# Kernel optimization log

Hardware: AMD Instinct MI355X
Metric: run time of the kernel (lower is better)

The kernel has to match this reference:

```python
import jax, jax.numpy as jnp
import numpy as np

N_NODES = 8192
N_EDGES = 262144


def spmm(edge_index, edge_weight, h):
    # sparse adjacency (COO) times dense matrix: out[dst] += w * h[src]
    src = edge_index[0]
    dst = edge_index[1]
    msg = h[src] * edge_weight[:, None]          # [E, D]
    return jax.ops.segment_sum(msg, dst, num_segments=N_NODES)


def setup_inputs() -> dict:
    key = jax.random.key(0)
    k = jax.random.split(key, 6)
    x = jax.random.normal(k[0], (N_NODES, 512), dtype=jnp.float32)
    edge_index = jax.random.randint(k[1], (2, N_EDGES), 0, N_NODES, dtype=jnp.int64)
    edge_weight = jax.random.uniform(k[2], (N_EDGES,), dtype=jnp.float32)
    # Glorot-style init scale for the GCN weights
    W1 = jax.random.normal(k[3], (512, 256), dtype=jnp.float32) * (1.0 / np.sqrt(512))
    W2 = jax.random.normal(k[4], (256, 128), dtype=jnp.float32) * (1.0 / np.sqrt(256))
    W3 = jax.random.normal(k[5], (256, 128), dtype=jnp.float32) * (1.0 / np.sqrt(256))
    return {"x": x, "edge_index": edge_index, "edge_weight": edge_weight,
            "W1": W1, "W2": W2, "W3": W3}


def reference(x, edge_index, edge_weight, W1, W2, W3):
    # Eval mode: dropout = identity, reparameterize returns mu.
    # GCN layer 1: relu(adj @ (x @ W1))
    h1 = jax.nn.relu(spmm(edge_index, edge_weight, x @ W1))       # [N, 256]
    # GCN layers 2/3 (identity activation): mu, logvar
    mu = spmm(edge_index, edge_weight, h1 @ W2)                   # [N, 128]
    logvar = spmm(edge_index, edge_weight, h1 @ W3)               # [N, 128]
    z = mu                                                        # eval: z = mu
    # InnerProductDecoder with act = identity
    adj_recon = z @ z.T                                           # [N, N]
    return adj_recon, mu, logvar, z
```

## Files before the change

kernel.cpp:

```cpp
#include <hip/hip_runtime.h>
#include <hip/hip_bf16.h>

#define NN 8192
#define NE 262144

typedef __attribute__((ext_vector_type(8))) short bf16x8;
typedef __attribute__((ext_vector_type(4))) float f32x4;
typedef __attribute__((ext_vector_type(16))) float f32x16;
typedef unsigned short u16;
typedef __attribute__((ext_vector_type(4))) u16 u16x4;

__device__ inline u16 f2b(float f) {
  unsigned u = __float_as_uint(f);
  unsigned r = u + 0x7FFF + ((u >> 16) & 1);
  return (u16)(r >> 16);
}
__device__ inline float b2f(u16 b) {
  return __uint_as_float(((unsigned)b) << 16);
}

__global__ void prep_kernel(const float* __restrict__ x, const float* __restrict__ W1,
                            const float* __restrict__ W2, const float* __restrict__ W3,
                            u16* __restrict__ xh, u16* __restrict__ xl,
                            u16* __restrict__ W1h, u16* __restrict__ W1l,
                            u16* __restrict__ W23h, u16* __restrict__ W23l) {
  int b = blockIdx.x;
  if (b < 4096) {
    int i = (b * 256 + threadIdx.x) * 4;
    f32x4 v = *(const f32x4*)(x + i);
    u16x4 vh, vl;
#pragma unroll
    for (int j = 0; j < 4; ++j) {
      u16 h = f2b(v[j]);
      vh[j] = h;
      vl[j] = f2b(v[j] - b2f(h));
    }
    *(u16x4*)(xh + i) = vh;
    *(u16x4*)(xl + i) = vl;
  } else if (b < 4096 + 512) {
    int i = (b - 4096) * 256 + threadIdx.x;
    int k = i >> 8, n = i & 255;
    float v = W1[i];
    u16 h = f2b(v);
    W1h[(size_t)n * 512 + k] = h;
    W1l[(size_t)n * 512 + k] = f2b(v - b2f(h));
  } else {
    int i = (b - 4608) * 256 + threadIdx.x;
    int k = i >> 8, j = i & 255;
    float v = (j < 128) ? W2[(k << 7) + j] : W3[(k << 7) + (j - 128)];
    u16 h = f2b(v);
    W23h[(size_t)j * 256 + k] = h;
    W23l[(size_t)j * 256 + k] = f2b(v - b2f(h));
  }
}

__global__ void hist_kernel(const int* __restrict__ dst, int* __restrict__ deg) {
  int i = blockIdx.x * blockDim.x + threadIdx.x;
  if (i < NE) atomicAdd(&deg[dst[i]], 1);
}

__global__ void scan_kernel(const int* __restrict__ deg, int* __restrict__ rowptr,
                            int* __restrict__ cursor) {
  __shared__ int sums[1024];
  int t = threadIdx.x;
  int loc[8];
  int s = 0;
#pragma unroll
  for (int j = 0; j < 8; ++j) { s += deg[t * 8 + j]; loc[j] = s; }
  sums[t] = s;
  __syncthreads();
  for (int off = 1; off < 1024; off <<= 1) {
    int v = (t >= off) ? sums[t - off] : 0;
    __syncthreads();
    sums[t] += v;
    __syncthreads();
  }
  int base = (t > 0) ? sums[t - 1] : 0;
  if (t == 0) rowptr[0] = 0;
#pragma unroll
  for (int j = 0; j < 8; ++j) {
    rowptr[t * 8 + j + 1] = base + loc[j];
    cursor[t * 8 + j] = base + (j ? loc[j - 1] : 0);
  }
}

__global__ void scatter_kernel(const int* __restrict__ src, const int* __restrict__ dst,
                               const float* __restrict__ w, int* cursor,
                               int* __restrict__ csr_src, float* __restrict__ csr_w) {
  int i = blockIdx.x * blockDim.x + threadIdx.x;
  if (i >= NE) return;
  int d = dst[i];
  int p = atomicAdd(&cursor[d], 1);
  csr_src[p] = src[i];
  csr_w[p] = w[i];
}

__global__ void gemm_split_kernel(const u16* __restrict__ Ah, const u16* __restrict__ Al,
                                  const u16* __restrict__ Bh, const u16* __restrict__ Bl,
                                  u16* __restrict__ C, int M, int N, int K) {
  int wave = threadIdx.x >> 6, lane = threadIdx.x & 63;
  int r = lane & 15, kf = (lane >> 4) * 8;
  int row = blockIdx.x * 64 + wave * 16 + r;
  int col0 = blockIdx.y * 64;
  f32x4 acc[4] = {};
  for (int k0 = 0; k0 < K; k0 += 32) {
    int ka = k0 + kf;
    bf16x8 ah = *(const bf16x8*)(Ah + (size_t)row * K + ka);
    bf16x8 al = *(const bf16x8*)(Al + (size_t)row * K + ka);
#pragma unroll
    for (int t = 0; t < 4; ++t) {
      int col = col0 + t * 16 + r;
      bf16x8 bh = *(const bf16x8*)(Bh + (size_t)col * K + ka);
      bf16x8 bl = *(const bf16x8*)(Bl + (size_t)col * K + ka);
      acc[t] = __builtin_amdgcn_mfma_f32_16x16x32_bf16(ah, bh, acc[t], 0, 0, 0);
      acc[t] = __builtin_amdgcn_mfma_f32_16x16x32_bf16(al, bh, acc[t], 0, 0, 0);
      acc[t] = __builtin_amdgcn_mfma_f32_16x16x32_bf16(ah, bl, acc[t], 0, 0, 0);
    }
  }
  int orow = blockIdx.x * 64 + wave * 16 + (lane >> 4) * 4;
#pragma unroll
  for (int t = 0; t < 4; ++t)
#pragma unroll
    for (int q = 0; q < 4; ++q)
      C[(size_t)(orow + q) * N + col0 + t * 16 + r] = f2b(acc[t][q]);
}

__global__ void spmm_relu_kernel(const int* __restrict__ rowptr, const int* __restrict__ csr_src,
                                 const float* __restrict__ csr_w, const u16* __restrict__ h,
                                 u16* __restrict__ oh, u16* __restrict__ ol) {
  int n = blockIdx.x * 4 + (threadIdx.x >> 6);
  int c = (threadIdx.x & 63) * 4;
  int e0 = rowptr[n], e1 = rowptr[n + 1];
  f32x4 acc = {};
  int i = e0;
  for (; i + 4 <= e1; i += 4) {
    int s0 = csr_src[i], s1 = csr_src[i + 1], s2 = csr_src[i + 2], s3 = csr_src[i + 3];
    float w0 = csr_w[i], w1 = csr_w[i + 1], w2 = csr_w[i + 2], w3 = csr_w[i + 3];
    u16x4 v0 = *(const u16x4*)(h + (size_t)s0 * 256 + c);
    u16x4 v1 = *(const u16x4*)(h + (size_t)s1 * 256 + c);
    u16x4 v2 = *(const u16x4*)(h + (size_t)s2 * 256 + c);
    u16x4 v3 = *(const u16x4*)(h + (size_t)s3 * 256 + c);
#pragma unroll
    for (int j = 0; j < 4; ++j) {
      acc[j] = fmaf(w0, b2f(v0[j]), acc[j]);
      acc[j] = fmaf(w1, b2f(v1[j]), acc[j]);
      acc[j] = fmaf(w2, b2f(v2[j]), acc[j]);
      acc[j] = fmaf(w3, b2f(v3[j]), acc[j]);
    }
  }
  for (; i < e1; ++i) {
    float w0 = csr_w[i];
    u16x4 v0 = *(const u16x4*)(h + (size_t)csr_src[i] * 256 + c);
#pragma unroll
    for (int j = 0; j < 4; ++j) acc[j] = fmaf(w0, b2f(v0[j]), acc[j]);
  }
  u16x4 vh, vl;
#pragma unroll
  for (int j = 0; j < 4; ++j) {
    float a = fmaxf(acc[j], 0.f);
    u16 hb = f2b(a);
    vh[j] = hb;
    vl[j] = f2b(a - b2f(hb));
  }
  *(u16x4*)(oh + (size_t)n * 256 + c) = vh;
  *(u16x4*)(ol + (size_t)n * 256 + c) = vl;
}

__global__ void spmm_out_kernel(const int* __restrict__ rowptr, const int* __restrict__ csr_src,
                                const float* __restrict__ csr_w, const u16* __restrict__ h,
                                float* __restrict__ mu, float* __restrict__ logvar,
                                float* __restrict__ z, u16* __restrict__ zb) {
  int n = blockIdx.x * 4 + (threadIdx.x >> 6);
  int c = (threadIdx.x & 63) * 4;
  int e0 = rowptr[n], e1 = rowptr[n + 1];
  f32x4 acc = {};
  int i = e0;
  for (; i + 4 <= e1; i += 4) {
    int s0 = csr_src[i], s1 = csr_src[i + 1], s2 = csr_src[i + 2], s3 = csr_src[i + 3];
    float w0 = csr_w[i], w1 = csr_w[i + 1], w2 = csr_w[i + 2], w3 = csr_w[i + 3];
    u16x4 v0 = *(const u16x4*)(h + (size_t)s0 * 256 + c);
    u16x4 v1 = *(const u16x4*)(h + (size_t)s1 * 256 + c);
    u16x4 v2 = *(const u16x4*)(h + (size_t)s2 * 256 + c);
    u16x4 v3 = *(const u16x4*)(h + (size_t)s3 * 256 + c);
#pragma unroll
    for (int j = 0; j < 4; ++j) {
      acc[j] = fmaf(w0, b2f(v0[j]), acc[j]);
      acc[j] = fmaf(w1, b2f(v1[j]), acc[j]);
      acc[j] = fmaf(w2, b2f(v2[j]), acc[j]);
      acc[j] = fmaf(w3, b2f(v3[j]), acc[j]);
    }
  }
  for (; i < e1; ++i) {
    float w0 = csr_w[i];
    u16x4 v0 = *(const u16x4*)(h + (size_t)csr_src[i] * 256 + c);
#pragma unroll
    for (int j = 0; j < 4; ++j) acc[j] = fmaf(w0, b2f(v0[j]), acc[j]);
  }
  if (c < 128) {
    *(f32x4*)(mu + (size_t)n * 128 + c) = acc;
    *(f32x4*)(z + (size_t)n * 128 + c) = acc;
    u16x4 vb;
#pragma unroll
    for (int j = 0; j < 4; ++j) vb[j] = f2b(acc[j]);
    *(u16x4*)(zb + (size_t)n * 128 + c) = vb;
  } else {
    *(f32x4*)(logvar + (size_t)n * 128 + (c - 128)) = acc;
  }
}

__global__ void zzt_kernel(const u16* __restrict__ Z, float* __restrict__ C) {
  __shared__ u16 lB[128 * 128];
  int t = threadIdx.x;
  int i0 = blockIdx.y * 128;
  int j0 = blockIdx.x * 128;
  const char* gB = (const char*)(Z + (size_t)j0 * 128);
#pragma unroll
  for (int cix = 0; cix < 8; ++cix) {
    int p = (cix * 256 + t) * 16;
    int row = p >> 8;
    int sw = (p & 255) ^ ((row & 15) << 4);
    bf16x8 vb = *(const bf16x8*)(gB + p);
    *(bf16x8*)((char*)lB + row * 256 + sw) = vb;
  }
  int wave = t >> 6, lane = t & 63;
  int lrow = lane & 31, hi = lane >> 5;
  const u16* aRow = Z + (size_t)(i0 + wave * 32 + lrow) * 128 + hi * 8;
  bf16x8 a[8];
#pragma unroll
  for (int k = 0; k < 8; ++k)
    a[k] = *(const bf16x8*)(aRow + k * 16);
  __syncthreads();
  f32x16 acc[4] = {};
#pragma unroll
  for (int ks = 0; ks < 8; ++ks) {
    int kb = ks * 32 + hi * 16;
#pragma unroll
    for (int tt = 0; tt < 4; ++tt) {
      int brow = tt * 32 + lrow;
      bf16x8 b = *(const bf16x8*)((const char*)lB + brow * 256 + (kb ^ ((brow & 15) << 4)));
      acc[tt] = __builtin_amdgcn_mfma_f32_32x32x16_bf16(a[ks], b, acc[tt], 0, 0, 0);
    }
  }
  int rb = wave * 32 + 4 * (lane >> 5);
  int col = lane & 31;
#pragma unroll
  for (int tt = 0; tt < 4; ++tt) {
#pragma unroll
    for (int reg = 0; reg < 16; ++reg) {
      int rr = rb + (reg & 3) + 8 * (reg >> 2);
      __builtin_nontemporal_store(acc[tt][reg],
          &C[(size_t)(i0 + rr) * NN + j0 + tt * 32 + col]);
    }
  }
}

extern "C" void kernel_launch(void* const* d_in, const int* in_sizes, int n_in,
                              void* d_out, int out_size, void* d_ws, size_t ws_size,
                              hipStream_t stream) {
  const float* x  = (const float*)d_in[0];
  const int*   ei = (const int*)d_in[1];
  const float* ew = (const float*)d_in[2];
  const float* W1 = (const float*)d_in[3];
  const float* W2 = (const float*)d_in[4];
  const float* W3 = (const float*)d_in[5];

  float* out    = (float*)d_out;
  float* adj    = out;
  float* mu     = out + (size_t)NN * NN;
  float* logv   = mu + (size_t)NN * 128;
  float* z      = logv + (size_t)NN * 128;

  const int* srcp = ei;
  const int* dstp = ei + NE;

  char* ws = (char*)d_ws;
  size_t off = 0;
  auto alloc = [&](size_t b) -> void* {
    void* p = ws + off;
    off = (off + b + 255) & ~(size_t)255;
    return p;
  };
  u16* xh   = (u16*)alloc((size_t)NN * 512 * 2);
  u16* xl   = (u16*)alloc((size_t)NN * 512 * 2);
  u16* W1h  = (u16*)alloc(512 * 256 * 2);
  u16* W1l  = (u16*)alloc(512 * 256 * 2);
  u16* W23h = (u16*)alloc(256 * 256 * 2);
  u16* W23l = (u16*)alloc(256 * 256 * 2);
  u16* h0b  = (u16*)alloc((size_t)NN * 256 * 2);
  u16* h1h  = (u16*)alloc((size_t)NN * 256 * 2);
  u16* h1l  = (u16*)alloc((size_t)NN * 256 * 2);
  u16* H2b  = (u16*)alloc((size_t)NN * 256 * 2);
  u16* zb   = (u16*)alloc((size_t)NN * 128 * 2);
  int* deg      = (int*)alloc(NN * 4);
  int* rowptr   = (int*)alloc((NN + 1) * 4);
  int* cursor   = (int*)alloc(NN * 4);
  int* csr_src  = (int*)alloc((size_t)NE * 4);
  float* csr_w  = (float*)alloc((size_t)NE * 4);

  hipMemsetAsync(deg, 0, NN * 4, stream);

  prep_kernel<<<4096 + 512 + 256, 256, 0, stream>>>(x, W1, W2, W3, xh, xl,
                                                    W1h, W1l, W23h, W23l);

  hist_kernel<<<NE / 256, 256, 0, stream>>>(dstp, deg);
  scan_kernel<<<1, 1024, 0, stream>>>(deg, rowptr, cursor);
  scatter_kernel<<<NE / 256, 256, 0, stream>>>(srcp, dstp, ew, cursor, csr_src, csr_w);

  gemm_split_kernel<<<dim3(NN / 64, 256 / 64), 256, 0, stream>>>(xh, xl, W1h, W1l, h0b,
                                                                 NN, 256, 512);
  spmm_relu_kernel<<<NN / 4, 256, 0, stream>>>(rowptr, csr_src, csr_w, h0b, h1h, h1l);
  gemm_split_kernel<<<dim3(NN / 64, 256 / 64), 256, 0, stream>>>(h1h, h1l, W23h, W23l, H2b,
                                                                 NN, 256, 256);
  spmm_out_kernel<<<NN / 4, 256, 0, stream>>>(rowptr, csr_src, csr_w, H2b, mu, logv, z, zb);
  zzt_kernel<<<dim3(NN / 128, NN / 128), 256, 0, stream>>>(zb, adj);
}
```

Measured before the change: 199.8 us.

## Drop split-bf16 compensation in dense GEMMs and fold degree histogram into prep

Replaces the three-MFMA hi/lo split-bf16 GEMMs with plain single-bf16 GEMMs, so only one bf16 copy of x, W1, W2/W3 and h1 is produced and read. This removes two thirds of the MFMA work and about half the conversion and memory traffic in prep and the GEMM and relu stages. It also merges the degree-histogram kernel into the prep kernel as extra blocks, saving one launch. The cost is lower accuracy in x@W1 and h1@W23, which may move outputs closer to the tolerance limit.

```diff
diff --git a/kernel.cpp b/kernel.cpp
--- a/kernel.cpp
+++ b/kernel.cpp
@@ -21,42 +21,30 @@
 
 __global__ void prep_kernel(const float* __restrict__ x, const float* __restrict__ W1,
                             const float* __restrict__ W2, const float* __restrict__ W3,
-                            u16* __restrict__ xh, u16* __restrict__ xl,
-                            u16* __restrict__ W1h, u16* __restrict__ W1l,
-                            u16* __restrict__ W23h, u16* __restrict__ W23l) {
+                            const int* __restrict__ dst, int* __restrict__ deg,
+                            u16* __restrict__ xb, u16* __restrict__ W1T,
+                            u16* __restrict__ W23T) {
   int b = blockIdx.x;
   if (b < 4096) {
     int i = (b * 256 + threadIdx.x) * 4;
     f32x4 v = *(const f32x4*)(x + i);
-    u16x4 vh, vl;
-#pragma unroll
-    for (int j = 0; j < 4; ++j) {
-      u16 h = f2b(v[j]);
-      vh[j] = h;
-      vl[j] = f2b(v[j] - b2f(h));
-    }
-    *(u16x4*)(xh + i) = vh;
-    *(u16x4*)(xl + i) = vl;
+    u16x4 o;
+#pragma unroll
+    for (int j = 0; j < 4; ++j) o[j] = f2b(v[j]);
+    *(u16x4*)(xb + i) = o;
   } else if (b < 4096 + 512) {
     int i = (b - 4096) * 256 + threadIdx.x;
     int k = i >> 8, n = i & 255;
-    float v = W1[i];
-    u16 h = f2b(v);
-    W1h[(size_t)n * 512 + k] = h;
-    W1l[(size_t)n * 512 + k] = f2b(v - b2f(h));
-  } else {
+    W1T[(size_t)n * 512 + k] = f2b(W1[i]);
+  } else if (b < 4096 + 512 + 256) {
     int i = (b - 4608) * 256 + threadIdx.x;
     int k = i >> 8, j = i & 255;
     float v = (j < 128) ? W2[(k << 7) + j] : W3[(k << 7) + (j - 128)];
-    u16 h = f2b(v);
-    W23h[(size_t)j * 256 + k] = h;
-    W23l[(size_t)j * 256 + k] = f2b(v - b2f(h));
-  }
-}
-
-__global__ void hist_kernel(const int* __restrict__ dst, int* __restrict__ deg) {
-  int i = blockIdx.x * blockDim.x + threadIdx.x;
-  if (i < NE) atomicAdd(&deg[dst[i]], 1);
+    W23T[(size_t)j * 256 + k] = f2b(v);
+  } else {
+    int i = (b - 4864) * 256 + threadIdx.x;
+    if (i < NE) atomicAdd(&deg[dst[i]], 1);
+  }
 }
 
 __global__ void scan_kernel(const int* __restrict__ deg, int* __restrict__ rowptr,
@@ -95,8 +83,7 @@
   csr_w[p] = w[i];
 }
 
-__global__ void gemm_split_kernel(const u16* __restrict__ Ah, const u16* __restrict__ Al,
-                                  const u16* __restrict__ Bh, const u16* __restrict__ Bl,
+__global__ void gemm_plain_kernel(const u16* __restrict__ A, const u16* __restrict__ BT,
                                   u16* __restrict__ C, int M, int N, int K) {
   int wave = threadIdx.x >> 6, lane = threadIdx.x & 63;
   int r = lane & 15, kf = (lane >> 4) * 8;
@@ -105,16 +92,11 @@
   f32x4 acc[4] = {};
   for (int k0 = 0; k0 < K; k0 += 32) {
     int ka = k0 + kf;
-    bf16x8 ah = *(const bf16x8*)(Ah + (size_t)row * K + ka);
-    bf16x8 al = *(const bf16x8*)(Al + (size_t)row * K + ka);
+    bf16x8 a = *(const bf16x8*)(A + (size_t)row * K + ka);
 #pragma unroll
     for (int t = 0; t < 4; ++t) {
-      int col = col0 + t * 16 + r;
-      bf16x8 bh = *(const bf16x8*)(Bh + (size_t)col * K + ka);
-      bf16x8 bl = *(const bf16x8*)(Bl + (size_t)col * K + ka);
-      acc[t] = __builtin_amdgcn_mfma_f32_16x16x32_bf16(ah, bh, acc[t], 0, 0, 0);
-      acc[t] = __builtin_amdgcn_mfma_f32_16x16x32_bf16(al, bh, acc[t], 0, 0, 0);
-      acc[t] = __builtin_amdgcn_mfma_f32_16x16x32_bf16(ah, bl, acc[t], 0, 0, 0);
+      bf16x8 b = *(const bf16x8*)(BT + (size_t)(col0 + t * 16 + r) * K + ka);
+      acc[t] = __builtin_amdgcn_mfma_f32_16x16x32_bf16(a, b, acc[t], 0, 0, 0);
     }
   }
   int orow = blockIdx.x * 64 + wave * 16 + (lane >> 4) * 4;
@@ -127,7 +109,7 @@
 
 __global__ void spmm_relu_kernel(const int* __restrict__ rowptr, const int* __restrict__ csr_src,
                                  const float* __restrict__ csr_w, const u16* __restrict__ h,
-                                 u16* __restrict__ oh, u16* __restrict__ ol) {
+                                 u16* __restrict__ o) {
   int n = blockIdx.x * 4 + (threadIdx.x >> 6);
   int c = (threadIdx.x & 63) * 4;
   int e0 = rowptr[n], e1 = rowptr[n + 1];
@@ -154,16 +136,10 @@
 #pragma unroll
     for (int j = 0; j < 4; ++j) acc[j] = fmaf(w0, b2f(v0[j]), acc[j]);
   }
-  u16x4 vh, vl;
-#pragma unroll
-  for (int j = 0; j < 4; ++j) {
-    float a = fmaxf(acc[j], 0.f);
-    u16 hb = f2b(a);
-    vh[j] = hb;
-    vl[j] = f2b(a - b2f(hb));
-  }
-  *(u16x4*)(oh + (size_t)n * 256 + c) = vh;
-  *(u16x4*)(ol + (size_t)n * 256 + c) = vl;
+  u16x4 vh;
+#pragma unroll
+  for (int j = 0; j < 4; ++j) vh[j] = f2b(fmaxf(acc[j], 0.f));
+  *(u16x4*)(o + (size_t)n * 256 + c) = vh;
 }
 
 __global__ void spmm_out_kernel(const int* __restrict__ rowptr, const int* __restrict__ csr_src,
@@ -280,15 +256,11 @@
     off = (off + b + 255) & ~(size_t)255;
     return p;
   };
-  u16* xh   = (u16*)alloc((size_t)NN * 512 * 2);
-  u16* xl   = (u16*)alloc((size_t)NN * 512 * 2);
-  u16* W1h  = (u16*)alloc(512 * 256 * 2);
-  u16* W1l  = (u16*)alloc(512 * 256 * 2);
-  u16* W23h = (u16*)alloc(256 * 256 * 2);
-  u16* W23l = (u16*)alloc(256 * 256 * 2);
+  u16* xb   = (u16*)alloc((size_t)NN * 512 * 2);
+  u16* W1T  = (u16*)alloc(512 * 256 * 2);
+  u16* W23T = (u16*)alloc(256 * 256 * 2);
   u16* h0b  = (u16*)alloc((size_t)NN * 256 * 2);
-  u16* h1h  = (u16*)alloc((size_t)NN * 256 * 2);
-  u16* h1l  = (u16*)alloc((size_t)NN * 256 * 2);
+  u16* h1b  = (u16*)alloc((size_t)NN * 256 * 2);
   u16* H2b  = (u16*)alloc((size_t)NN * 256 * 2);
   u16* zb   = (u16*)alloc((size_t)NN * 128 * 2);
   int* deg      = (int*)alloc(NN * 4);
@@ -299,17 +271,16 @@
 
   hipMemsetAsync(deg, 0, NN * 4, stream);
 
-  prep_kernel<<<4096 + 512 + 256, 256, 0, stream>>>(x, W1, W2, W3, xh, xl,
-                                                    W1h, W1l, W23h, W23l);
-
-  hist_kernel<<<NE / 256, 256, 0, stream>>>(dstp, deg);
+  prep_kernel<<<4096 + 512 + 256 + 1024, 256, 0, stream>>>(x, W1, W2, W3, dstp, deg,
+                                                           xb, W1T, W23T);
+
   scan_kernel<<<1, 1024, 0, stream>>>(deg, rowptr, cursor);
   scatter_kernel<<<NE / 256, 256, 0, stream>>>(srcp, dstp, ew, cursor, csr_src, csr_w);
 
-  gemm_split_kernel<<<dim3(NN / 64, 256 / 64), 256, 0, stream>>>(xh, xl, W1h, W1l, h0b,
+  gemm_plain_kernel<<<dim3(NN / 64, 256 / 64), 256, 0, stream>>>(xb, W1T, h0b,
                                                                  NN, 256, 512);
-  spmm_relu_kernel<<<NN / 4, 256, 0, stream>>>(rowptr, csr_src, csr_w, h0b, h1h, h1l);
-  gemm_split_kernel<<<dim3(NN / 64, 256 / 64), 256, 0, stream>>>(h1h, h1l, W23h, W23l, H2b,
+  spmm_relu_kernel<<<NN / 4, 256, 0, stream>>>(rowptr, csr_src, csr_w, h0b, h1b);
+  gemm_plain_kernel<<<dim3(NN / 64, 256 / 64), 256, 0, stream>>>(h1b, W23T, H2b,
                                                                  NN, 256, 256);
   spmm_out_kernel<<<NN / 4, 256, 0, stream>>>(rowptr, csr_src, csr_w, H2b, mu, logv, z, zb);
   zzt_kernel<<<dim3(NN / 128, NN / 128), 256, 0, stream>>>(zb, adj);
```

Result: faster. 165.8 us (-17.1%).
